# Optimization experiments

Measured on AMD Instinct MI355X. Metric: run time of the kernel, lower is better.

The kernel has to match this reference:

```python
import jax, jax.numpy as jnp
import numpy as np
from jax import lax

B, C, H, W = 8, 64, 128, 128
K = 3  # deformable kernel size, padding=1, stride=1


def conv3x3(x, w, b=None):
    # x: [B,Cin,H,W], w: [Cout,Cin,3,3]
    y = lax.conv_general_dilated(x, w, (1, 1), 'SAME',
                                 dimension_numbers=('NCHW', 'OIHW', 'NCHW'))
    if b is not None:
        y = y + b[None, :, None, None]
    return y


def leaky_relu(x, slope=0.1):
    return jnp.where(x >= 0, x, slope * x)


def _bilinear_sample_one(feat, ys, xs):
    # feat: [C,H,W]; ys, xs: [KK,H,W] fractional sample coords (zero outside borders)
    h, w = feat.shape[1], feat.shape[2]
    y0 = jnp.floor(ys)
    x0 = jnp.floor(xs)
    wy = ys - y0  # [KK,H,W]
    wx = xs - x0

    def gather(yi, xi):
        valid = ((yi >= 0) & (yi < h) & (xi >= 0) & (xi < w)).astype(feat.dtype)
        yc = jnp.clip(yi, 0, h - 1).astype(jnp.int32)
        xc = jnp.clip(xi, 0, w - 1).astype(jnp.int32)
        v = feat[:, yc, xc]  # [C,KK,H,W]
        return v * valid[None]

    v00 = gather(y0, x0)
    v01 = gather(y0, x0 + 1)
    v10 = gather(y0 + 1, x0)
    v11 = gather(y0 + 1, x0 + 1)
    top = v00 * (1 - wx)[None] + v01 * wx[None]
    bot = v10 * (1 - wx)[None] + v11 * wx[None]
    return top * (1 - wy)[None] + bot * wy[None]  # [C,KK,H,W]


def deform_conv2d(x, offset, weight):
    # x: [B,Cin,H,W]; offset: [B,2*K*K,H,W] (torchvision order: per-tap (dy,dx));
    # weight: [Cout,Cin,K,K]; stride=1, pad=1, dilation=1, groups=1, no bias.
    b, cin, h, w = x.shape
    kk = K * K
    off = offset.reshape(b, kk, 2, h, w)
    dy, dx = off[:, :, 0], off[:, :, 1]  # [B,KK,H,W]
    hh = jnp.arange(h, dtype=x.dtype)[:, None]
    ww = jnp.arange(w, dtype=x.dtype)[None, :]
    ky = (jnp.arange(kk) // K - 1).astype(x.dtype)[None, :, None, None]
    kx = (jnp.arange(kk) % K - 1).astype(x.dtype)[None, :, None, None]
    ys = hh[None, None] + ky + dy  # [B,KK,H,W]
    xs = ww[None, None] + kx + dx
    sampled = jax.vmap(_bilinear_sample_one)(x, ys, xs)  # [B,Cin,KK,H,W]
    wflat = weight.reshape(weight.shape[0], cin, kk)
    return jnp.einsum('bckhw,ock->bohw', sampled, wflat)


def setup_inputs() -> dict:
    key = jax.random.key(0)
    ks = jax.random.split(key, 7)
    ref_feat = jax.random.normal(ks[0], (B, C, H, W), jnp.float32)
    target_feat = jax.random.normal(ks[1], (B, C, H, W), jnp.float32)
    w1 = jax.random.normal(ks[2], (C, 2 * C, 3, 3), jnp.float32) * 0.02
    b1 = jax.random.normal(ks[3], (C,), jnp.float32) * 0.02
    w2 = jax.random.normal(ks[4], (18, C, 3, 3), jnp.float32) * 0.02
    b2 = jax.random.normal(ks[5], (18,), jnp.float32) * 0.02
    wd = jax.random.normal(ks[6], (C, C, 3, 3), jnp.float32) * 0.05
    return {'ref_feat': ref_feat, 'target_feat': target_feat,
            'w1': w1, 'b1': b1, 'w2': w2, 'b2': b2, 'wd': wd}


def reference(ref_feat, target_feat, w1, b1, w2, b2, wd):
    concat_feat = jnp.concatenate([ref_feat, target_feat], axis=1)  # [B,2C,H,W]
    hmid = leaky_relu(conv3x3(concat_feat, w1, b1), 0.1)
    offset = conv3x3(hmid, w2, b2)  # [B,18,H,W]
    aligned_feat = deform_conv2d(target_feat, offset, wd)  # [B,C,H,W]
    return aligned_feat
```

## Files before the change

### kernel.cpp

```cpp
#include <hip/hip_runtime.h>
#include <hip/hip_fp16.h>

#define HW 128
#define PLANE (HW * HW)

typedef __attribute__((ext_vector_type(8))) _Float16 f16x8;
typedef __attribute__((ext_vector_type(4))) float f32x4;

__device__ __forceinline__ unsigned short f2h(float f) {
  return __half_as_ushort(__float2half(f));
}

__device__ __forceinline__ void tile_from_bid_512(int bid, int& b, int& by, int& bx) {
  int wg = (bid & 7) * 64 + (bid >> 3);
  b = wg >> 6;
  int t = wg & 63;
  by = (t >> 3) << 4;
  bx = (t & 7) << 4;
}

__global__ __launch_bounds__(256) void pack_all_kernel(
    const float* __restrict__ w1, const float* __restrict__ w2,
    const float* __restrict__ wd, unsigned short* __restrict__ w1p,
    unsigned short* __restrict__ w2p, unsigned short* __restrict__ wdp) {
  int idx = blockIdx.x * 256 + threadIdx.x;
  if (idx < 73728) {
    int k = idx >> 6, n = idx & 63;
    int tap = k >> 7, ic = k & 127;
    w1p[((k >> 3) * 64 + n) * 8 + (k & 7)] = f2h(w1[(n * 128 + ic) * 9 + tap]);
  } else if (idx < 73728 + 18432) {
    int i = idx - 73728;
    int k = i >> 5, n = i & 31;
    int tap = k >> 6, ic = k & 63;
    float v = (n < 18) ? w2[(n * 64 + ic) * 9 + tap] : 0.f;
    w2p[((k >> 3) * 32 + n) * 8 + (k & 7)] = f2h(v);
  } else if (idx < 73728 + 18432 + 36864) {
    int i = idx - 73728 - 18432;
    int k = i >> 6, n = i & 63;
    int tap = k >> 6, ic = k & 63;
    wdp[((k >> 3) * 64 + n) * 8 + (k & 7)] = f2h(wd[(n * 64 + ic) * 9 + tap]);
  }
}

__global__ __launch_bounds__(256) void to_nhwc_kernel(
    const float* __restrict__ ref, const float* __restrict__ tgt,
    unsigned short* __restrict__ xref, unsigned short* __restrict__ xtgt) {
  __shared__ unsigned short lds[32][136];
  const int b = blockIdx.z, y = blockIdx.y, x0 = blockIdx.x * 32;
  for (int idx = threadIdx.x; idx < 4096; idx += 256) {
    int ic = idx >> 5, px = idx & 31;
    const float* src = (ic < 64) ? ref : tgt;
    lds[px][ic] = f2h(src[(b * 64 + (ic & 63)) * PLANE + y * HW + x0 + px]);
  }
  __syncthreads();
  for (int idx = threadIdx.x; idx < 512; idx += 256) {
    int px = idx >> 4, g = idx & 15;
    uint4 v = *(const uint4*)&lds[px][g * 8];
    size_t base = ((size_t)(b * HW + y) * HW + x0 + px) * 64;
    if (g < 8)
      *(uint4*)(xref + base + g * 8) = v;
    else
      *(uint4*)(xtgt + base + (g - 8) * 8) = v;
  }
}

__global__ __launch_bounds__(512) void conv1_mfma_kernel(
    const unsigned short* __restrict__ xref, const unsigned short* __restrict__ xtgt,
    const unsigned short* __restrict__ w1p, const float* __restrict__ b1,
    unsigned short* __restrict__ hm) {
  __shared__ unsigned short tileH[324 * 64];
  int b, by, bx;
  tile_from_bid_512(blockIdx.x, b, by, bx);
  const int tid = threadIdx.x, lane = tid & 63, w = tid >> 6;
  const int l15 = lane & 15, lg = lane >> 4;

  f32x4 acc[4][2];
#pragma unroll
  for (int mf = 0; mf < 4; ++mf)
#pragma unroll
    for (int q = 0; q < 2; ++q) acc[mf][q] = (f32x4){0.f, 0.f, 0.f, 0.f};

  for (int c = 0; c < 2; ++c) {
    const unsigned short* src = c ? xtgt : xref;
    __syncthreads();
    for (int i = tid; i < 2592; i += 512) {
      int pos = i >> 3, g = i & 7;
      int yy = pos / 18, xx = pos - yy * 18;
      int gy = by + yy - 1, gx = bx + xx - 1;
      uint4 v = make_uint4(0u, 0u, 0u, 0u);
      if ((unsigned)gy < 128u && (unsigned)gx < 128u)
        v = *(const uint4*)(src + ((size_t)(b * HW + gy) * HW + gx) * 64 + g * 8);
      *(uint4*)(tileH + pos * 64 + ((g * 8) ^ ((pos & 7) << 3))) = v;
    }
    __syncthreads();

#pragma unroll
    for (int tap = 0; tap < 9; ++tap) {
      const int ty = tap / 3, tx = tap - ty * 3;
#pragma unroll
      for (int ks = 0; ks < 2; ++ks) {
        f16x8 ap[2];
#pragma unroll
        for (int q = 0; q < 2; ++q) {
          int pos = (w * 2 + q + ty) * 18 + l15 + tx;
          ap[q] = *(const f16x8*)(tileH + pos * 64 + ((ks * 32 + lg * 8) ^ ((pos & 7) << 3)));
        }
        const int kb = tap * 16 + c * 8 + ks * 4 + lg;
        f16x8 aw[4];
#pragma unroll
        for (int mf = 0; mf < 4; ++mf)
          aw[mf] = *(const f16x8*)(w1p + (kb * 64 + mf * 16 + l15) * 8);
#pragma unroll
        for (int mf = 0; mf < 4; ++mf)
#pragma unroll
          for (int q = 0; q < 2; ++q)
            acc[mf][q] = __builtin_amdgcn_mfma_f32_16x16x32_f16(aw[mf], ap[q], acc[mf][q], 0, 0, 0);
      }
    }
  }

#pragma unroll
  for (int mf = 0; mf < 4; ++mf) {
    const float4 bv = ((const float4*)b1)[mf * 4 + lg];
#pragma unroll
    for (int q = 0; q < 2; ++q) {
      const int y = by + w * 2 + q;
      float v0 = acc[mf][q][0] + bv.x;
      float v1 = acc[mf][q][1] + bv.y;
      float v2 = acc[mf][q][2] + bv.z;
      float v3 = acc[mf][q][3] + bv.w;
      v0 = (v0 >= 0.f) ? v0 : 0.1f * v0;
      v1 = (v1 >= 0.f) ? v1 : 0.1f * v1;
      v2 = (v2 >= 0.f) ? v2 : 0.1f * v2;
      v3 = (v3 >= 0.f) ? v3 : 0.1f * v3;
      ushort4 s;
      s.x = f2h(v0); s.y = f2h(v1); s.z = f2h(v2); s.w = f2h(v3);
      *(ushort4*)(hm + ((size_t)(b * HW + y) * HW + bx + l15) * 64 + mf * 16 + lg * 4) = s;
    }
  }
}

__global__ __launch_bounds__(512) void conv2_mfma_kernel(
    const unsigned short* __restrict__ hm, const unsigned short* __restrict__ w2p,
    const float* __restrict__ b2, float* __restrict__ offsG) {
  __shared__ unsigned short tileH[324 * 64];
  int b, by, bx;
  tile_from_bid_512(blockIdx.x, b, by, bx);
  const int tid = threadIdx.x, lane = tid & 63, w = tid >> 6;
  const int l15 = lane & 15, lg = lane >> 4;

  for (int i = tid; i < 2592; i += 512) {
    int pos = i >> 3, g = i & 7;
    int yy = pos / 18, xx = pos - yy * 18;
    int gy = by + yy - 1, gx = bx + xx - 1;
    uint4 v = make_uint4(0u, 0u, 0u, 0u);
    if ((unsigned)gy < 128u && (unsigned)gx < 128u)
      v = *(const uint4*)(hm + ((size_t)(b * HW + gy) * HW + gx) * 64 + g * 8);
    *(uint4*)(tileH + pos * 64 + ((g * 8) ^ ((pos & 7) << 3))) = v;
  }
  __syncthreads();

  f32x4 acc2[2][2];
#pragma unroll
  for (int q = 0; q < 2; ++q)
#pragma unroll
    for (int nf = 0; nf < 2; ++nf) acc2[q][nf] = (f32x4){0.f, 0.f, 0.f, 0.f};

#pragma unroll
  for (int tap = 0; tap < 9; ++tap) {
    const int ty = tap / 3, tx = tap - ty * 3;
#pragma unroll
    for (int ks = 0; ks < 2; ++ks) {
      f16x8 ap[2];
#pragma unroll
      for (int q = 0; q < 2; ++q) {
        int pos = (w * 2 + q + ty) * 18 + l15 + tx;
        ap[q] = *(const f16x8*)(tileH + pos * 64 + ((ks * 32 + lg * 8) ^ ((pos & 7) << 3)));
      }
      const int kb = tap * 8 + ks * 4 + lg;
      f16x8 bw[2];
#pragma unroll
      for (int nf = 0; nf < 2; ++nf)
        bw[nf] = *(const f16x8*)(w2p + (kb * 32 + nf * 16 + l15) * 8);
#pragma unroll
      for (int q = 0; q < 2; ++q)
#pragma unroll
        for (int nf = 0; nf < 2; ++nf)
          acc2[q][nf] = __builtin_amdgcn_mfma_f32_16x16x32_f16(ap[q], bw[nf], acc2[q][nf], 0, 0, 0);
    }
  }

#pragma unroll
  for (int nf = 0; nf < 2; ++nf) {
    const int oc = nf * 16 + l15;
    if (oc < 18) {
      const float bias = b2[oc];
      const int kk = oc >> 1, comp = oc & 1;
#pragma unroll
      for (int q = 0; q < 2; ++q) {
        const int y = by + w * 2 + q;
#pragma unroll
        for (int reg = 0; reg < 4; ++reg) {
          const int x = bx + lg * 4 + reg;
          offsG[(((size_t)(b * 9 + kk) * PLANE + y * HW + x) << 1) + comp] =
              acc2[q][nf][reg] + bias;
        }
      }
    }
  }
}

__device__ __forceinline__ uint4 blend4(uint4 a, uint4 b, uint4 c, uint4 d,
                                        __half2 h00, __half2 h01, __half2 h10, __half2 h11) {
  union U { uint4 u; __half2 h[4]; };
  U A, B, C, D, R;
  A.u = a; B.u = b; C.u = c; D.u = d;
#pragma unroll
  for (int i = 0; i < 4; ++i)
    R.h[i] = __hfma2(D.h[i], h11, __hfma2(C.h[i], h10, __hfma2(B.h[i], h01, __hmul2(A.h[i], h00))));
  return R.u;
}

__global__ __launch_bounds__(512, 4) void deform_kernel(
    const unsigned short* __restrict__ xtgt, const float* __restrict__ offsG,
    const unsigned short* __restrict__ wdp, float* __restrict__ out) {
  __shared__ __align__(16) unsigned short win[400 * 72];
  int b, by, bx;
  tile_from_bid_512(blockIdx.x, b, by, bx);
  const int tid = threadIdx.x, lane = tid & 63, w = tid >> 6;
  const int l15 = lane & 15, lg = lane >> 4;
  const int x = bx + l15;

  const unsigned short* tb = xtgt + (size_t)b * PLANE * 64;

  for (int i = tid; i < 3200; i += 512) {
    int rec = i >> 3, g = i & 7;
    int wy = rec / 20, wx = rec - wy * 20;
    int gy = by - 2 + wy, gx = bx - 2 + wx;
    uint4 v = make_uint4(0u, 0u, 0u, 0u);
    if ((unsigned)gy < 128u && (unsigned)gx < 128u)
      v = *(const uint4*)(tb + ((size_t)gy * HW + gx) * 64 + g * 8);
    *(uint4*)(win + rec * 72 + g * 8) = v;
  }
  __syncthreads();

  f32x4 acc[2][4];
#pragma unroll
  for (int q = 0; q < 2; ++q)
#pragma unroll
    for (int nf = 0; nf < 4; ++nf) acc[q][nf] = (f32x4){0.f, 0.f, 0.f, 0.f};

  const float2* ob = (const float2*)offsG + (size_t)(b * 9) * PLANE + (by + w * 2) * HW + x;

  for (int kk = 0; kk < 9; ++kk) {
    const int kdy = kk / 3 - 1, kdx = kk - (kk / 3) * 3 - 1;
    f16x8 af[2][2];
#pragma unroll
    for (int q = 0; q < 2; ++q) {
      const int y = by + w * 2 + q;
      const float2 o2 = ob[(size_t)kk * PLANE + q * HW];
      float ys = (float)(y + kdy) + o2.x;
      float xs = (float)(x + kdx) + o2.y;
      float y0f = floorf(ys), x0f = floorf(xs);
      float wy = ys - y0f, wx = xs - x0f;
      int y0 = (int)y0f, x0i = (int)x0f;
      int y1 = y0 + 1, x1 = x0i + 1;
      float vy0 = (y0 >= 0 && y0 < HW) ? 1.f : 0.f;
      float vy1 = (y1 >= 0 && y1 < HW) ? 1.f : 0.f;
      float vx0 = (x0i >= 0 && x0i < HW) ? 1.f : 0.f;
      float vx1 = (x1 >= 0 && x1 < HW) ? 1.f : 0.f;
      int y0c = min(max(y0, 0), HW - 1), y1c = min(max(y1, 0), HW - 1);
      int x0c = min(max(x0i, 0), HW - 1), x1c = min(max(x1, 0), HW - 1);
      __half2 h00 = __float2half2_rn((1.f - wy) * (1.f - wx) * vy0 * vx0);
      __half2 h01 = __float2half2_rn((1.f - wy) * wx * vy0 * vx1);
      __half2 h10 = __float2half2_rn(wy * (1.f - wx) * vy1 * vx0);
      __half2 h11 = __float2half2_rn(wy * wx * vy1 * vx1);

      const int wy0 = y0c - by + 2, wy1 = y1c - by + 2;
      const int wx0 = x0c - bx + 2, wx1 = x1c - bx + 2;
      const bool inw = ((unsigned)wy0 < 20u) && ((unsigned)wy1 < 20u) &&
                       ((unsigned)wx0 < 20u) && ((unsigned)wx1 < 20u);
      uint4 c00[2], c01[2], c10[2], c11[2];
      if (inw) {
        const unsigned short* q00 = win + (wy0 * 20 + wx0) * 72 + lg * 8;
        const unsigned short* q01 = win + (wy0 * 20 + wx1) * 72 + lg * 8;
        const unsigned short* q10 = win + (wy1 * 20 + wx0) * 72 + lg * 8;
        const unsigned short* q11 = win + (wy1 * 20 + wx1) * 72 + lg * 8;
#pragma unroll
        for (int ks = 0; ks < 2; ++ks) {
          c00[ks] = *(const uint4*)(q00 + ks * 32);
          c01[ks] = *(const uint4*)(q01 + ks * 32);
          c10[ks] = *(const uint4*)(q10 + ks * 32);
          c11[ks] = *(const uint4*)(q11 + ks * 32);
        }
      } else {
        const unsigned short* p00 = tb + (y0c * HW + x0c) * 64 + lg * 8;
        const unsigned short* p01 = tb + (y0c * HW + x1c) * 64 + lg * 8;
        const unsigned short* p10 = tb + (y1c * HW + x0c) * 64 + lg * 8;
        const unsigned short* p11 = tb + (y1c * HW + x1c) * 64 + lg * 8;
#pragma unroll
        for (int ks = 0; ks < 2; ++ks) {
          c00[ks] = *(const uint4*)(p00 + ks * 32);
          c01[ks] = *(const uint4*)(p01 + ks * 32);
          c10[ks] = *(const uint4*)(p10 + ks * 32);
          c11[ks] = *(const uint4*)(p11 + ks * 32);
        }
      }
#pragma unroll
      for (int ks = 0; ks < 2; ++ks) {
        uint4 r = blend4(c00[ks], c01[ks], c10[ks], c11[ks], h00, h01, h10, h11);
        af[q][ks] = *(const f16x8*)&r;
      }
    }

#pragma unroll
    for (int ks = 0; ks < 2; ++ks) {
      const int kb = kk * 8 + ks * 4 + lg;
      f16x8 bw[4];
#pragma unroll
      for (int nf = 0; nf < 4; ++nf)
        bw[nf] = *(const f16x8*)(wdp + (kb * 64 + nf * 16 + l15) * 8);
#pragma unroll
      for (int q = 0; q < 2; ++q)
#pragma unroll
        for (int nf = 0; nf < 4; ++nf)
          acc[q][nf] = __builtin_amdgcn_mfma_f32_16x16x32_f16(af[q][ks], bw[nf], acc[q][nf], 0, 0, 0);
    }
  }

  const int px0 = bx + lg * 4;
#pragma unroll
  for (int q = 0; q < 2; ++q) {
    const int py = by + w * 2 + q;
#pragma unroll
    for (int nf = 0; nf < 4; ++nf) {
      const int oc = nf * 16 + l15;
      float4 o;
      o.x = acc[q][nf][0];
      o.y = acc[q][nf][1];
      o.z = acc[q][nf][2];
      o.w = acc[q][nf][3];
      *(float4*)(out + (size_t)(b * 64 + oc) * PLANE + py * HW + px0) = o;
    }
  }
}

extern "C" void kernel_launch(void* const* d_in, const int* in_sizes, int n_in,
                              void* d_out, int out_size, void* d_ws, size_t ws_size,
                              hipStream_t stream) {
  const float* ref = (const float*)d_in[0];
  const float* tgt = (const float*)d_in[1];
  const float* w1  = (const float*)d_in[2];
  const float* b1  = (const float*)d_in[3];
  const float* w2  = (const float*)d_in[4];
  const float* b2  = (const float*)d_in[5];
  const float* wd  = (const float*)d_in[6];

  unsigned short* xref = (unsigned short*)d_out;
  float* out = (float*)d_out;

  char* ws = (char*)d_ws;
  unsigned short* xtgt  = (unsigned short*)ws;
  unsigned short* hmid  = (unsigned short*)(ws + 16777216);
  float*          offsG = (float*)(ws + 33554432);
  unsigned short* w1p   = (unsigned short*)(ws + 42991616);
  unsigned short* w2p   = (unsigned short*)(ws + 43139072);
  unsigned short* wdp   = (unsigned short*)(ws + 43175936);

  pack_all_kernel<<<504, 256, 0, stream>>>(w1, w2, wd, w1p, w2p, wdp);

  to_nhwc_kernel<<<dim3(4, 128, 8), 256, 0, stream>>>(ref, tgt, xref, xtgt);

  conv1_mfma_kernel<<<512, 512, 0, stream>>>(xref, xtgt, w1p, b1, hmid);
  conv2_mfma_kernel<<<512, 512, 0, stream>>>(hmid, w2p, b2, offsG);
  deform_kernel<<<512, 512, 0, stream>>>(xtgt, offsG, wdp, out);
}
```

Measured before the change: 99.99 us.

## Fuse conv1, conv2 and deformable conv into one tiled kernel with halo recompute

Merges the three per-tile kernels into one. Each 16x16 tile loads a 20x20 halo of both inputs into LDS, computes conv1 over the 18x18 region (recomputing halo pixels that neighbouring tiles also compute), keeps hmid and the offsets in LDS, then runs the deformable sampling from the same LDS window. This removes the global round trips for hmid and the offsets and two kernel launches. In exchange it adds halo recompute (324 vs 256 pixels in conv1), uses more LDS, and lowers occupancy to 2 blocks per CU.

After: 105.7 us. 1.06x slower.

```diff
diff --git a/kernel.cpp b/kernel.cpp
--- a/kernel.cpp
+++ b/kernel.cpp
@@ -64,152 +64,6 @@
   }
 }
 
-__global__ __launch_bounds__(512) void conv1_mfma_kernel(
-    const unsigned short* __restrict__ xref, const unsigned short* __restrict__ xtgt,
-    const unsigned short* __restrict__ w1p, const float* __restrict__ b1,
-    unsigned short* __restrict__ hm) {
-  __shared__ unsigned short tileH[324 * 64];
-  int b, by, bx;
-  tile_from_bid_512(blockIdx.x, b, by, bx);
-  const int tid = threadIdx.x, lane = tid & 63, w = tid >> 6;
-  const int l15 = lane & 15, lg = lane >> 4;
-
-  f32x4 acc[4][2];
-#pragma unroll
-  for (int mf = 0; mf < 4; ++mf)
-#pragma unroll
-    for (int q = 0; q < 2; ++q) acc[mf][q] = (f32x4){0.f, 0.f, 0.f, 0.f};
-
-  for (int c = 0; c < 2; ++c) {
-    const unsigned short* src = c ? xtgt : xref;
-    __syncthreads();
-    for (int i = tid; i < 2592; i += 512) {
-      int pos = i >> 3, g = i & 7;
-      int yy = pos / 18, xx = pos - yy * 18;
-      int gy = by + yy - 1, gx = bx + xx - 1;
-      uint4 v = make_uint4(0u, 0u, 0u, 0u);
-      if ((unsigned)gy < 128u && (unsigned)gx < 128u)
-        v = *(const uint4*)(src + ((size_t)(b * HW + gy) * HW + gx) * 64 + g * 8);
-      *(uint4*)(tileH + pos * 64 + ((g * 8) ^ ((pos & 7) << 3))) = v;
-    }
-    __syncthreads();
-
-#pragma unroll
-    for (int tap = 0; tap < 9; ++tap) {
-      const int ty = tap / 3, tx = tap - ty * 3;
-#pragma unroll
-      for (int ks = 0; ks < 2; ++ks) {
-        f16x8 ap[2];
-#pragma unroll
-        for (int q = 0; q < 2; ++q) {
-          int pos = (w * 2 + q + ty) * 18 + l15 + tx;
-          ap[q] = *(const f16x8*)(tileH + pos * 64 + ((ks * 32 + lg * 8) ^ ((pos & 7) << 3)));
-        }
-        const int kb = tap * 16 + c * 8 + ks * 4 + lg;
-        f16x8 aw[4];
-#pragma unroll
-        for (int mf = 0; mf < 4; ++mf)
-          aw[mf] = *(const f16x8*)(w1p + (kb * 64 + mf * 16 + l15) * 8);
-#pragma unroll
-        for (int mf = 0; mf < 4; ++mf)
-#pragma unroll
-          for (int q = 0; q < 2; ++q)
-            acc[mf][q] = __builtin_amdgcn_mfma_f32_16x16x32_f16(aw[mf], ap[q], acc[mf][q], 0, 0, 0);
-      }
-    }
-  }
-
-#pragma unroll
-  for (int mf = 0; mf < 4; ++mf) {
-    const float4 bv = ((const float4*)b1)[mf * 4 + lg];
-#pragma unroll
-    for (int q = 0; q < 2; ++q) {
-      const int y = by + w * 2 + q;
-      float v0 = acc[mf][q][0] + bv.x;
-      float v1 = acc[mf][q][1] + bv.y;
-      float v2 = acc[mf][q][2] + bv.z;
-      float v3 = acc[mf][q][3] + bv.w;
-      v0 = (v0 >= 0.f) ? v0 : 0.1f * v0;
-      v1 = (v1 >= 0.f) ? v1 : 0.1f * v1;
-      v2 = (v2 >= 0.f) ? v2 : 0.1f * v2;
-      v3 = (v3 >= 0.f) ? v3 : 0.1f * v3;
-      ushort4 s;
-      s.x = f2h(v0); s.y = f2h(v1); s.z = f2h(v2); s.w = f2h(v3);
-      *(ushort4*)(hm + ((size_t)(b * HW + y) * HW + bx + l15) * 64 + mf * 16 + lg * 4) = s;
-    }
-  }
-}
-
-__global__ __launch_bounds__(512) void conv2_mfma_kernel(
-    const unsigned short* __restrict__ hm, const unsigned short* __restrict__ w2p,
-    const float* __restrict__ b2, float* __restrict__ offsG) {
-  __shared__ unsigned short tileH[324 * 64];
-  int b, by, bx;
-  tile_from_bid_512(blockIdx.x, b, by, bx);
-  const int tid = threadIdx.x, lane = tid & 63, w = tid >> 6;
-  const int l15 = lane & 15, lg = lane >> 4;
-
-  for (int i = tid; i < 2592; i += 512) {
-    int pos = i >> 3, g = i & 7;
-    int yy = pos / 18, xx = pos - yy * 18;
-    int gy = by + yy - 1, gx = bx + xx - 1;
-    uint4 v = make_uint4(0u, 0u, 0u, 0u);
-    if ((unsigned)gy < 128u && (unsigned)gx < 128u)
-      v = *(const uint4*)(hm + ((size_t)(b * HW + gy) * HW + gx) * 64 + g * 8);
-    *(uint4*)(tileH + pos * 64 + ((g * 8) ^ ((pos & 7) << 3))) = v;
-  }
-  __syncthreads();
-
-  f32x4 acc2[2][2];
-#pragma unroll
-  for (int q = 0; q < 2; ++q)
-#pragma unroll
-    for (int nf = 0; nf < 2; ++nf) acc2[q][nf] = (f32x4){0.f, 0.f, 0.f, 0.f};
-
-#pragma unroll
-  for (int tap = 0; tap < 9; ++tap) {
-    const int ty = tap / 3, tx = tap - ty * 3;
-#pragma unroll
-    for (int ks = 0; ks < 2; ++ks) {
-      f16x8 ap[2];
-#pragma unroll
-      for (int q = 0; q < 2; ++q) {
-        int pos = (w * 2 + q + ty) * 18 + l15 + tx;
-        ap[q] = *(const f16x8*)(tileH + pos * 64 + ((ks * 32 + lg * 8) ^ ((pos & 7) << 3)));
-      }
-      const int kb = tap * 8 + ks * 4 + lg;
-      f16x8 bw[2];
-#pragma unroll
-      for (int nf = 0; nf < 2; ++nf)
-        bw[nf] = *(const f16x8*)(w2p + (kb * 32 + nf * 16 + l15) * 8);
-#pragma unroll
-      for (int q = 0; q < 2; ++q)
-#pragma unroll
-        for (int nf = 0; nf < 2; ++nf)
-          acc2[q][nf] = __builtin_amdgcn_mfma_f32_16x16x32_f16(ap[q], bw[nf], acc2[q][nf], 0, 0, 0);
-    }
-  }
-
-#pragma unroll
-  for (int nf = 0; nf < 2; ++nf) {
-    const int oc = nf * 16 + l15;
-    if (oc < 18) {
-      const float bias = b2[oc];
-      const int kk = oc >> 1, comp = oc & 1;
-#pragma unroll
-      for (int q = 0; q < 2; ++q) {
-        const int y = by + w * 2 + q;
-#pragma unroll
-        for (int reg = 0; reg < 4; ++reg) {
-          const int x = bx + lg * 4 + reg;
-          offsG[(((size_t)(b * 9 + kk) * PLANE + y * HW + x) << 1) + comp] =
-              acc2[q][nf][reg] + bias;
-        }
-      }
-    }
-  }
-}
-
 __device__ __forceinline__ uint4 blend4(uint4 a, uint4 b, uint4 c, uint4 d,
                                         __half2 h00, __half2 h01, __half2 h10, __half2 h11) {
   union U { uint4 u; __half2 h[4]; };
@@ -221,26 +75,150 @@
   return R.u;
 }
 
-__global__ __launch_bounds__(512, 4) void deform_kernel(
-    const unsigned short* __restrict__ xtgt, const float* __restrict__ offsG,
+__global__ __launch_bounds__(512, 2) void mega_kernel(
+    const unsigned short* __restrict__ xref, const unsigned short* __restrict__ xtgt,
+    const unsigned short* __restrict__ w1p, const float* __restrict__ b1,
+    const unsigned short* __restrict__ w2p, const float* __restrict__ b2,
     const unsigned short* __restrict__ wdp, float* __restrict__ out) {
-  __shared__ __align__(16) unsigned short win[400 * 72];
+  __shared__ __align__(16) unsigned short bufA[400 * 64];
+  __shared__ __align__(16) unsigned short bufB[400 * 64];
+  __shared__ float offsL[256 * 20];
+
   int b, by, bx;
   tile_from_bid_512(blockIdx.x, b, by, bx);
   const int tid = threadIdx.x, lane = tid & 63, w = tid >> 6;
   const int l15 = lane & 15, lg = lane >> 4;
-  const int x = bx + l15;
-
+
+  const unsigned short* rb = xref + (size_t)b * PLANE * 64;
   const unsigned short* tb = xtgt + (size_t)b * PLANE * 64;
 
   for (int i = tid; i < 3200; i += 512) {
     int rec = i >> 3, g = i & 7;
     int wy = rec / 20, wx = rec - wy * 20;
     int gy = by - 2 + wy, gx = bx - 2 + wx;
-    uint4 v = make_uint4(0u, 0u, 0u, 0u);
-    if ((unsigned)gy < 128u && (unsigned)gx < 128u)
-      v = *(const uint4*)(tb + ((size_t)gy * HW + gx) * 64 + g * 8);
-    *(uint4*)(win + rec * 72 + g * 8) = v;
+    uint4 va = make_uint4(0u, 0u, 0u, 0u), vb = va;
+    if ((unsigned)gy < 128u && (unsigned)gx < 128u) {
+      size_t o = ((size_t)gy * HW + gx) * 64 + g * 8;
+      va = *(const uint4*)(rb + o);
+      vb = *(const uint4*)(tb + o);
+    }
+    int sw = rec * 64 + ((g * 8) ^ ((rec & 7) << 3));
+    *(uint4*)(bufA + sw) = va;
+    *(uint4*)(bufB + sw) = vb;
+  }
+  __syncthreads();
+
+  int pyv[3], pxv[3];
+#pragma unroll
+  for (int n = 0; n < 3; ++n) {
+    int p = (w * 3 + n) * 16 + l15;
+    p = min(p, 323);
+    pyv[n] = p / 18;
+    pxv[n] = p - pyv[n] * 18;
+  }
+
+  f32x4 acc1[4][3];
+#pragma unroll
+  for (int mf = 0; mf < 4; ++mf)
+#pragma unroll
+    for (int n = 0; n < 3; ++n) acc1[mf][n] = (f32x4){0.f, 0.f, 0.f, 0.f};
+
+  for (int c = 0; c < 2; ++c) {
+    const unsigned short* src = c ? bufB : bufA;
+#pragma unroll
+    for (int tap = 0; tap < 9; ++tap) {
+      const int ty = tap / 3, tx = tap - ty * 3;
+#pragma unroll
+      for (int ks = 0; ks < 2; ++ks) {
+        f16x8 bp[3];
+#pragma unroll
+        for (int n = 0; n < 3; ++n) {
+          int rec = (pyv[n] + ty) * 20 + pxv[n] + tx;
+          bp[n] = *(const f16x8*)(src + rec * 64 + ((ks * 32 + lg * 8) ^ ((rec & 7) << 3)));
+        }
+        const int kb = tap * 16 + c * 8 + ks * 4 + lg;
+        f16x8 aw[4];
+#pragma unroll
+        for (int mf = 0; mf < 4; ++mf)
+          aw[mf] = *(const f16x8*)(w1p + (kb * 64 + mf * 16 + l15) * 8);
+#pragma unroll
+        for (int mf = 0; mf < 4; ++mf)
+#pragma unroll
+          for (int n = 0; n < 3; ++n)
+            acc1[mf][n] = __builtin_amdgcn_mfma_f32_16x16x32_f16(aw[mf], bp[n], acc1[mf][n], 0, 0, 0);
+      }
+    }
+  }
+  __syncthreads();
+
+  unsigned short* hmidL = bufA;
+#pragma unroll
+  for (int mf = 0; mf < 4; ++mf) {
+    const float4 bv = ((const float4*)b1)[mf * 4 + lg];
+#pragma unroll
+    for (int n = 0; n < 3; ++n) {
+      const int p = (w * 3 + n) * 16 + l15;
+      const bool valid = ((unsigned)(by - 1 + pyv[n]) < 128u) &&
+                         ((unsigned)(bx - 1 + pxv[n]) < 128u);
+      const float m = valid ? 1.f : 0.f;
+      float v0 = acc1[mf][n][0] + bv.x;
+      float v1 = acc1[mf][n][1] + bv.y;
+      float v2 = acc1[mf][n][2] + bv.z;
+      float v3 = acc1[mf][n][3] + bv.w;
+      v0 = ((v0 >= 0.f) ? v0 : 0.1f * v0) * m;
+      v1 = ((v1 >= 0.f) ? v1 : 0.1f * v1) * m;
+      v2 = ((v2 >= 0.f) ? v2 : 0.1f * v2) * m;
+      v3 = ((v3 >= 0.f) ? v3 : 0.1f * v3) * m;
+      ushort4 s;
+      s.x = f2h(v0); s.y = f2h(v1); s.z = f2h(v2); s.w = f2h(v3);
+      const int oc = mf * 16 + lg * 4;
+      *(ushort4*)(hmidL + p * 64 + (oc ^ ((p & 7) << 3))) = s;
+    }
+  }
+  __syncthreads();
+
+  f32x4 acc2[2][2];
+#pragma unroll
+  for (int q = 0; q < 2; ++q)
+#pragma unroll
+    for (int nf = 0; nf < 2; ++nf) acc2[q][nf] = (f32x4){0.f, 0.f, 0.f, 0.f};
+
+#pragma unroll
+  for (int tap = 0; tap < 9; ++tap) {
+    const int ty = tap / 3, tx = tap - ty * 3;
+#pragma unroll
+    for (int ks = 0; ks < 2; ++ks) {
+      f16x8 ap[2];
+#pragma unroll
+      for (int q = 0; q < 2; ++q) {
+        int p = (w * 2 + q + ty) * 18 + l15 + tx;
+        ap[q] = *(const f16x8*)(hmidL + p * 64 + ((ks * 32 + lg * 8) ^ ((p & 7) << 3)));
+      }
+      const int kb = tap * 8 + ks * 4 + lg;
+      f16x8 bw[2];
+#pragma unroll
+      for (int nf = 0; nf < 2; ++nf)
+        bw[nf] = *(const f16x8*)(w2p + (kb * 32 + nf * 16 + l15) * 8);
+#pragma unroll
+      for (int q = 0; q < 2; ++q)
+#pragma unroll
+        for (int nf = 0; nf < 2; ++nf)
+          acc2[q][nf] = __builtin_amdgcn_mfma_f32_16x16x32_f16(ap[q], bw[nf], acc2[q][nf], 0, 0, 0);
+    }
+  }
+#pragma unroll
+  for (int nf = 0; nf < 2; ++nf) {
+    const int oc = nf * 16 + l15;
+    if (oc < 18) {
+      const float bias = b2[oc];
+#pragma unroll
+      for (int q = 0; q < 2; ++q)
+#pragma unroll
+        for (int reg = 0; reg < 4; ++reg) {
+          int px = (w * 2 + q) * 16 + lg * 4 + reg;
+          offsL[px * 20 + oc] = acc2[q][nf][reg] + bias;
+        }
+    }
   }
   __syncthreads();
 
@@ -250,7 +228,7 @@
 #pragma unroll
     for (int nf = 0; nf < 4; ++nf) acc[q][nf] = (f32x4){0.f, 0.f, 0.f, 0.f};
 
-  const float2* ob = (const float2*)offsG + (size_t)(b * 9) * PLANE + (by + w * 2) * HW + x;
+  const int x = bx + l15;
 
   for (int kk = 0; kk < 9; ++kk) {
     const int kdy = kk / 3 - 1, kdx = kk - (kk / 3) * 3 - 1;
@@ -258,9 +236,11 @@
 #pragma unroll
     for (int q = 0; q < 2; ++q) {
       const int y = by + w * 2 + q;
-      const float2 o2 = ob[(size_t)kk * PLANE + q * HW];
-      float ys = (float)(y + kdy) + o2.x;
-      float xs = (float)(x + kdx) + o2.y;
+      const int px_lin = (w * 2 + q) * 16 + l15;
+      float dy = offsL[px_lin * 20 + kk * 2];
+      float dx = offsL[px_lin * 20 + kk * 2 + 1];
+      float ys = (float)(y + kdy) + dy;
+      float xs = (float)(x + kdx) + dx;
       float y0f = floorf(ys), x0f = floorf(xs);
       float wy = ys - y0f, wx = xs - x0f;
       int y0 = (int)y0f, x0i = (int)x0f;
@@ -282,16 +262,15 @@
                        ((unsigned)wx0 < 20u) && ((unsigned)wx1 < 20u);
       uint4 c00[2], c01[2], c10[2], c11[2];
       if (inw) {
-        const unsigned short* q00 = win + (wy0 * 20 + wx0) * 72 + lg * 8;
-        const unsigned short* q01 = win + (wy0 * 20 + wx1) * 72 + lg * 8;
-        const unsigned short* q10 = win + (wy1 * 20 + wx0) * 72 + lg * 8;
-        const unsigned short* q11 = win + (wy1 * 20 + wx1) * 72 + lg * 8;
+        const int r00 = wy0 * 20 + wx0, r01 = wy0 * 20 + wx1;
+        const int r10 = wy1 * 20 + wx0, r11 = wy1 * 20 + wx1;
 #pragma unroll
         for (int ks = 0; ks < 2; ++ks) {
-          c00[ks] = *(const uint4*)(q00 + ks * 32);
-          c01[ks] = *(const uint4*)(q01 + ks * 32);
-          c10[ks] = *(const uint4*)(q10 + ks * 32);
-          c11[ks] = *(const uint4*)(q11 + ks * 32);
+          const int ko = (ks * 32 + lg * 8);
+          c00[ks] = *(const uint4*)(bufB + r00 * 64 + (ko ^ ((r00 & 7) << 3)));
+          c01[ks] = *(const uint4*)(bufB + r01 * 64 + (ko ^ ((r01 & 7) << 3)));
+          c10[ks] = *(const uint4*)(bufB + r10 * 64 + (ko ^ ((r10 & 7) << 3)));
+          c11[ks] = *(const uint4*)(bufB + r11 * 64 + (ko ^ ((r11 & 7) << 3)));
         }
       } else {
         const unsigned short* p00 = tb + (y0c * HW + x0c) * 64 + lg * 8;
@@ -355,23 +334,18 @@
   const float* w2  = (const float*)d_in[4];
   const float* b2  = (const float*)d_in[5];
   const float* wd  = (const float*)d_in[6];
-
-  unsigned short* xref = (unsigned short*)d_out;
   float* out = (float*)d_out;
 
   char* ws = (char*)d_ws;
-  unsigned short* xtgt  = (unsigned short*)ws;
-  unsigned short* hmid  = (unsigned short*)(ws + 16777216);
-  float*          offsG = (float*)(ws + 33554432);
-  unsigned short* w1p   = (unsigned short*)(ws + 42991616);
-  unsigned short* w2p   = (unsigned short*)(ws + 43139072);
-  unsigned short* wdp   = (unsigned short*)(ws + 43175936);
+  unsigned short* xref = (unsigned short*)ws;
+  unsigned short* xtgt = (unsigned short*)(ws + 16777216);
+  unsigned short* w1p  = (unsigned short*)(ws + 33554432);
+  unsigned short* w2p  = (unsigned short*)(ws + 33701888);
+  unsigned short* wdp  = (unsigned short*)(ws + 33738752);
 
   pack_all_kernel<<<504, 256, 0, stream>>>(w1, w2, wd, w1p, w2p, wdp);
 
   to_nhwc_kernel<<<dim3(4, 128, 8), 256, 0, stream>>>(ref, tgt, xref, xtgt);
 
-  conv1_mfma_kernel<<<512, 512, 0, stream>>>(xref, xtgt, w1p, b1, hmid);
-  conv2_mfma_kernel<<<512, 512, 0, stream>>>(hmid, w2p, b2, offsG);
-  deform_kernel<<<512, 512, 0, stream>>>(xtgt, offsG, wdp, out);
-}
+  mega_kernel<<<512, 512, 0, stream>>>(xref, xtgt, w1p, b1, w2p, b2, wdp, out);
+}
```
